# Performance work log

Hardware: AMD Instinct MI355X
Metric: run time of the kernel (lower is better)

Reference implementation:

```python
import jax, jax.numpy as jnp
import numpy as np

N, E, D_IN, HID = 100000, 3200000, 256, 128
EPS = 1e-5  # BatchNorm1d default eps


def batchnorm(x, gamma, beta):
    # training-mode BatchNorm1d: batch stats, biased variance
    mu = x.mean(axis=0)
    var = ((x - mu) ** 2).mean(axis=0)
    return (x - mu) * jax.lax.rsqrt(var + EPS) * gamma + beta


def setup_inputs() -> dict:
    key = jax.random.key(0)
    ks = jax.random.split(key, 6)
    s_in = 1.0 / np.sqrt(D_IN)
    s_h = 1.0 / np.sqrt(HID)
    return {
        "x": jax.random.normal(ks[0], (N, D_IN), jnp.float32),
        "edge_index": jax.random.randint(ks[1], (2, E), 0, N),
        "W1": jax.random.uniform(ks[2], (D_IN, HID), jnp.float32, -s_in, s_in),
        "b1": jnp.zeros((HID,), jnp.float32),
        "g1": jnp.ones((HID,), jnp.float32),
        "be1": jnp.zeros((HID,), jnp.float32),
        "Wl": jax.random.uniform(ks[3], (HID, HID), jnp.float32, -s_h, s_h),
        "bl": jnp.zeros((HID,), jnp.float32),
        "Wr": jax.random.uniform(ks[4], (HID, HID), jnp.float32, -s_h, s_h),
        "g2": jnp.ones((HID,), jnp.float32),
        "be2": jnp.zeros((HID,), jnp.float32),
    }


def reference(x, edge_index, W1, b1, g1, be1, Wl, bl, Wr, g2, be2):
    # input_linear: Linear -> BatchNorm1d, then ReLU
    feat = jax.nn.relu(batchnorm(x @ W1 + b1, g1, be1))  # [N, HID]

    # SAGEConv: mean-aggregate source features at destinations
    src, dst = edge_index[0], edge_index[1]
    msg_sum = jax.ops.segment_sum(feat[src], dst, num_segments=N)       # [N, HID]
    deg = jax.ops.segment_sum(jnp.ones((E, 1), feat.dtype), dst, num_segments=N)
    mean = msg_sum / jnp.maximum(deg, 1.0)

    # out = lin_l(aggr) + lin_r(x); lin_l has bias, lin_r does not (PyG default)
    out = mean @ Wl + bl + feat @ Wr
    out_feat = batchnorm(out, g2, be2)
    return feat, out_feat
```

## Files before the change

### kernel.cpp

```cpp
#include <hip/hip_runtime.h>

#define NN 100000
#define NE 3200000
#define KD 256
#define HD 128
#define NB 782
#define CAP 4608

typedef __bf16 bf16x8 __attribute__((ext_vector_type(8)));
typedef float  f32x8  __attribute__((ext_vector_type(8)));
typedef float  f32x4  __attribute__((ext_vector_type(4)));
typedef float  f32x2  __attribute__((ext_vector_type(2)));
typedef unsigned u32x2 __attribute__((ext_vector_type(2)));
typedef unsigned u32x4 __attribute__((ext_vector_type(4)));

__device__ __forceinline__ f32x4 mfma16(bf16x8 a, bf16x8 b, f32x4 c) {
  return __builtin_amdgcn_mfma_f32_16x16x32_bf16(a, b, c, 0, 0, 0);
}

__global__ void prep_w(const float* __restrict__ W1, const float* __restrict__ Wl,
                       const float* __restrict__ Wr, __bf16* __restrict__ Bt1,
                       __bf16* __restrict__ Bt2, float* __restrict__ stats,
                       int* __restrict__ bucket_cur) {
  if (blockIdx.x == 0) {
    for (int i = threadIdx.x; i < 1024; i += 256) stats[i] = 0.f;
  } else if (blockIdx.x == 1) {
    for (int i = threadIdx.x; i < NB; i += 256) bucket_cur[i] = i * CAP;
  }
  int c = blockIdx.x;
  int k = threadIdx.x;
  Bt1[c * KD + k] = (__bf16)W1[k * HD + c];
  float w = (k < HD) ? Wl[k * HD + c] : Wr[(k - HD) * HD + c];
  Bt2[c * KD + k] = (__bf16)w;
}

__global__ __launch_bounds__(1024) void b_scatter(const int* __restrict__ src,
                                                  const int* __restrict__ dst,
                                                  int* __restrict__ bucket_cur,
                                                  unsigned* __restrict__ pairs) {
  __shared__ int h[NB];
  __shared__ int cur[NB];
  __shared__ int gbase[NB];
  for (int i = threadIdx.x; i < NB; i += 1024) { h[i] = 0; cur[i] = 0; }
  __syncthreads();
  int base = blockIdx.x * 12500;
  for (int i = threadIdx.x; i < 12500; i += 1024)
    atomicAdd(&h[dst[base + i] >> 7], 1);
  __syncthreads();
  for (int b = threadIdx.x; b < NB; b += 1024) {
    int c = h[b];
    gbase[b] = c ? atomicAdd(&bucket_cur[b], c) : 0;
  }
  __syncthreads();
  for (int i = threadIdx.x; i < 12500; i += 1024) {
    int d = dst[base + i];
    int s = src[base + i];
    int b = d >> 7;
    int r = atomicAdd(&cur[b], 1);
    pairs[gbase[b] + r] = ((unsigned)s << 7) | (unsigned)(d & 127);
  }
}

__global__ __launch_bounds__(256) void b_sort(const int* __restrict__ bucket_cur,
                                              unsigned* __restrict__ pc,
                                              int* __restrict__ row_start,
                                              int* __restrict__ row_cnt) {
  __shared__ unsigned sin[CAP];
  __shared__ unsigned sout[CAP];
  __shared__ int h[128], ex[128];
  int b = blockIdx.x;
  int n0 = b * CAP;
  int cnt = bucket_cur[b] - n0;
  if (cnt > CAP) cnt = CAP;
  if (threadIdx.x < 128) h[threadIdx.x] = 0;
  __syncthreads();
  for (int i = threadIdx.x; i < cnt; i += 256) {
    unsigned v = pc[n0 + i];
    sin[i] = v;
    atomicAdd(&h[v & 127], 1);
  }
  __syncthreads();
  if (threadIdx.x < 128) ex[threadIdx.x] = h[threadIdx.x];
  __syncthreads();
  for (int off = 1; off < 128; off <<= 1) {
    int u = 0;
    if (threadIdx.x < 128 && threadIdx.x >= off) u = ex[threadIdx.x - off];
    __syncthreads();
    if (threadIdx.x < 128) ex[threadIdx.x] += u;
    __syncthreads();
  }
  if (threadIdx.x < 128) {
    int c = h[threadIdx.x];
    int excl = ex[threadIdx.x] - c;
    int node = b * 128 + threadIdx.x;
    if (node < NN) {
      row_start[node] = n0 + excl;
      row_cnt[node] = c;
    }
    h[threadIdx.x] = excl;
  }
  __syncthreads();
  for (int i = threadIdx.x; i < cnt; i += 256) {
    unsigned v = sin[i];
    int r = atomicAdd(&h[v & 127], 1);
    sout[r] = v >> 7;
  }
  __syncthreads();
  for (int i = threadIdx.x; i < cnt; i += 256)
    pc[n0 + i] = sout[i];
}

__global__ __launch_bounds__(256, 2) void gemm_x(const float* __restrict__ A,
                                                 const __bf16* __restrict__ Bt,
                                                 float* __restrict__ C,
                                                 float* __restrict__ sumc,
                                                 float* __restrict__ sqc) {
  __shared__ __bf16 sB[HD * KD];
  __shared__ float lsum[HD], lsq[HD];
  int tid = threadIdx.x;
  if (tid < HD) { lsum[tid] = 0.f; lsq[tid] = 0.f; }
  int wave = tid >> 6, lane = tid & 63;
  int q = lane >> 4, m = lane & 15;
  int rowbase = blockIdx.x * 256 + wave * 64;
  for (int i = tid; i < HD * KD / 8; i += 256) {
    int r = i >> 5, g = i & 31;
    bf16x8 v = *(const bf16x8*)(Bt + (size_t)r * KD + (g << 3));
    *(bf16x8*)(&sB[r * KD + ((g ^ (r & 7)) << 3)]) = v;
  }
  bf16x8 areg[4][8];
#pragma unroll
  for (int g = 0; g < 4; ++g) {
    int r = rowbase + g * 16 + m;
    if (r > NN - 1) r = NN - 1;
    const float* pa = A + (size_t)r * KD + q * 8;
    f32x8 u[8];
#pragma unroll
    for (int k = 0; k < 8; ++k) u[k] = *(const f32x8*)(pa + k * 32);
#pragma unroll
    for (int k = 0; k < 8; ++k) areg[g][k] = __builtin_convertvector(u[k], bf16x8);
  }
  __syncthreads();
#pragma unroll
  for (int hh = 0; hh < 2; ++hh) {
    f32x4 acc[4][4];
    f32x4 z = {0.f, 0.f, 0.f, 0.f};
#pragma unroll
    for (int g = 0; g < 4; ++g)
#pragma unroll
      for (int t = 0; t < 4; ++t) acc[g][t] = z;
#pragma unroll
    for (int ks = 0; ks < 8; ++ks) {
      int gb = ks * 4 + q;
#pragma unroll
      for (int t = 0; t < 4; ++t) {
        int c = hh * 64 + t * 16 + m;
        bf16x8 bb = *(const bf16x8*)(&sB[c * KD + ((gb ^ (c & 7)) << 3)]);
#pragma unroll
        for (int g = 0; g < 4; ++g) acc[g][t] = mfma16(areg[g][ks], bb, acc[g][t]);
      }
    }
    float ps[4], pq2[4];
#pragma unroll
    for (int t = 0; t < 4; ++t) { ps[t] = 0.f; pq2[t] = 0.f; }
#pragma unroll
    for (int g = 0; g < 4; ++g)
#pragma unroll
      for (int rg = 0; rg < 4; ++rg) {
        int r = rowbase + g * 16 + q * 4 + rg;
        if (r < NN) {
          float* Cr = C + (size_t)r * HD + hh * 64 + m;
#pragma unroll
          for (int t = 0; t < 4; ++t) {
            float v = acc[g][t][rg];
            Cr[t * 16] = v;
            ps[t] += v;
            pq2[t] += v * v;
          }
        }
      }
#pragma unroll
    for (int t = 0; t < 4; ++t) {
      atomicAdd(&lsum[hh * 64 + t * 16 + m], ps[t]);
      atomicAdd(&lsq[hh * 64 + t * 16 + m], pq2[t]);
    }
  }
  __syncthreads();
  if (tid < HD) {
    atomicAdd(&sumc[tid], lsum[tid]);
    atomicAdd(&sqc[tid], lsq[tid]);
  }
}

__global__ __launch_bounds__(256, 2) void gemm_cat(const __bf16* __restrict__ A0,
                                                   const __bf16* __restrict__ A1,
                                                   const __bf16* __restrict__ Bt,
                                                   float* __restrict__ C,
                                                   float* __restrict__ sumc,
                                                   float* __restrict__ sqc) {
  __shared__ __bf16 sB[HD * KD];
  __shared__ float lsum[HD], lsq[HD];
  int tid = threadIdx.x;
  if (tid < HD) { lsum[tid] = 0.f; lsq[tid] = 0.f; }
  int wave = tid >> 6, lane = tid & 63;
  int q = lane >> 4, m = lane & 15;
  int rowbase = blockIdx.x * 256 + wave * 64;
  for (int i = tid; i < HD * KD / 8; i += 256) {
    int r = i >> 5, g = i & 31;
    bf16x8 v = *(const bf16x8*)(Bt + (size_t)r * KD + (g << 3));
    *(bf16x8*)(&sB[r * KD + ((g ^ (r & 7)) << 3)]) = v;
  }
  bf16x8 areg[4][8];
#pragma unroll
  for (int g = 0; g < 4; ++g) {
    int r = rowbase + g * 16 + m;
    if (r > NN - 1) r = NN - 1;
    const __bf16* p0 = A0 + (size_t)r * HD + q * 8;
    const __bf16* p1 = A1 + (size_t)r * HD + q * 8;
#pragma unroll
    for (int k = 0; k < 4; ++k) areg[g][k] = *(const bf16x8*)(p0 + k * 32);
#pragma unroll
    for (int k = 0; k < 4; ++k) areg[g][4 + k] = *(const bf16x8*)(p1 + k * 32);
  }
  __syncthreads();
#pragma unroll
  for (int hh = 0; hh < 2; ++hh) {
    f32x4 acc[4][4];
    f32x4 z = {0.f, 0.f, 0.f, 0.f};
#pragma unroll
    for (int g = 0; g < 4; ++g)
#pragma unroll
      for (int t = 0; t < 4; ++t) acc[g][t] = z;
#pragma unroll
    for (int ks = 0; ks < 8; ++ks) {
      int gb = ks * 4 + q;
#pragma unroll
      for (int t = 0; t < 4; ++t) {
        int c = hh * 64 + t * 16 + m;
        bf16x8 bb = *(const bf16x8*)(&sB[c * KD + ((gb ^ (c & 7)) << 3)]);
#pragma unroll
        for (int g = 0; g < 4; ++g) acc[g][t] = mfma16(areg[g][ks], bb, acc[g][t]);
      }
    }
    float ps[4], pq2[4];
#pragma unroll
    for (int t = 0; t < 4; ++t) { ps[t] = 0.f; pq2[t] = 0.f; }
#pragma unroll
    for (int g = 0; g < 4; ++g)
#pragma unroll
      for (int rg = 0; rg < 4; ++rg) {
        int r = rowbase + g * 16 + q * 4 + rg;
        if (r < NN) {
          float* Cr = C + (size_t)r * HD + hh * 64 + m;
#pragma unroll
          for (int t = 0; t < 4; ++t) {
            float v = acc[g][t][rg];
            Cr[t * 16] = v;
            ps[t] += v;
            pq2[t] += v * v;
          }
        }
      }
#pragma unroll
    for (int t = 0; t < 4; ++t) {
      atomicAdd(&lsum[hh * 64 + t * 16 + m], ps[t]);
      atomicAdd(&lsq[hh * 64 + t * 16 + m], pq2[t]);
    }
  }
  __syncthreads();
  if (tid < HD) {
    atomicAdd(&sumc[tid], lsum[tid]);
    atomicAdd(&sqc[tid], lsq[tid]);
  }
}

__global__ __launch_bounds__(256) void bn_apply(const float* __restrict__ X,
                                                const float* __restrict__ sumc,
                                                const float* __restrict__ sqc,
                                                const float* __restrict__ g,
                                                const float* __restrict__ be,
                                                float* __restrict__ outf,
                                                __bf16* __restrict__ outb,
                                                unsigned char* __restrict__ outq,
                                                int relu) {
  __shared__ float sc[HD], sh[HD];
  if (threadIdx.x < HD) {
    int c = threadIdx.x;
    float mu = sumc[c] * (1.0f / NN);
    float var = sqc[c] * (1.0f / NN) - mu * mu;
    float rs = rsqrtf(var + 1e-5f);
    float a = rs * g[c];
    sc[c] = a;
    sh[c] = be[c] - mu * a;
  }
  __syncthreads();
  size_t base = ((size_t)blockIdx.x * 256 + threadIdx.x) * 8;
  int c0 = (int)(base & (HD - 1));
  f32x4 x0 = *(const f32x4*)(X + base);
  f32x4 x1 = *(const f32x4*)(X + base + 4);
  float o[8];
#pragma unroll
  for (int j = 0; j < 8; ++j) {
    float xv = (j < 4) ? x0[j] : x1[j - 4];
    float v = xv * sc[c0 + j] + sh[c0 + j];
    if (relu) v = fmaxf(v, 0.f);
    o[j] = v;
  }
  f32x4 o0 = {o[0], o[1], o[2], o[3]};
  f32x4 o1 = {o[4], o[5], o[6], o[7]};
  *(f32x4*)(outf + base) = o0;
  *(f32x4*)(outf + base + 4) = o1;
  if (outb) {
    bf16x8 ob;
#pragma unroll
    for (int j = 0; j < 8; ++j) ob[j] = (__bf16)o[j];
    *(bf16x8*)(outb + base) = ob;
    int w0 = 0, w1 = 0;
    w0 = __builtin_amdgcn_cvt_pk_fp8_f32(o[0], o[1], w0, false);
    w0 = __builtin_amdgcn_cvt_pk_fp8_f32(o[2], o[3], w0, true);
    w1 = __builtin_amdgcn_cvt_pk_fp8_f32(o[4], o[5], w1, false);
    w1 = __builtin_amdgcn_cvt_pk_fp8_f32(o[6], o[7], w1, true);
    u32x2 qv = {(unsigned)w0, (unsigned)w1};
    *(u32x2*)(outq + base) = qv;
  }
}

__global__ __launch_bounds__(256) void aggregate(const int* __restrict__ row_start,
                                                 const int* __restrict__ row_cnt,
                                                 const unsigned* __restrict__ csr,
                                                 const unsigned char* __restrict__ featq,
                                                 __bf16* __restrict__ meanb) {
  int node = blockIdx.x * 4 + (threadIdx.x >> 6);
  if (node >= NN) return;
  int lane = threadIdx.x & 63;
  int sub = lane >> 3;
  int m = lane & 7;
  int s = row_start[node];
  int deg = row_cnt[node];
  int e = s + deg;
  f32x2 acc[8];
#pragma unroll
  for (int j = 0; j < 8; ++j) acc[j] = (f32x2){0.f, 0.f};
  const u32x4* rows = (const u32x4*)featq;
  for (int base = s; base < e; base += 64) {
    int nb = e - base;
    if (nb > 64) nb = 64;
    unsigned my = 0;
    if (lane < nb) my = csr[base + lane];
#pragma unroll
    for (int t = 0; t < 64; t += 8) {
      int slot = t + sub;
      unsigned sn = __shfl(my, slot, 64);
      if (slot < nb) {
        u32x4 v = rows[(size_t)sn * 8 + m];
        acc[0] += __builtin_amdgcn_cvt_pk_f32_fp8((int)v.x, false);
        acc[1] += __builtin_amdgcn_cvt_pk_f32_fp8((int)v.x, true);
        acc[2] += __builtin_amdgcn_cvt_pk_f32_fp8((int)v.y, false);
        acc[3] += __builtin_amdgcn_cvt_pk_f32_fp8((int)v.y, true);
        acc[4] += __builtin_amdgcn_cvt_pk_f32_fp8((int)v.z, false);
        acc[5] += __builtin_amdgcn_cvt_pk_f32_fp8((int)v.z, true);
        acc[6] += __builtin_amdgcn_cvt_pk_f32_fp8((int)v.w, false);
        acc[7] += __builtin_amdgcn_cvt_pk_f32_fp8((int)v.w, true);
      }
    }
  }
#pragma unroll
  for (int j = 0; j < 8; ++j) {
    acc[j].x += __shfl_xor(acc[j].x, 8, 64);
    acc[j].y += __shfl_xor(acc[j].y, 8, 64);
    acc[j].x += __shfl_xor(acc[j].x, 16, 64);
    acc[j].y += __shfl_xor(acc[j].y, 16, 64);
    acc[j].x += __shfl_xor(acc[j].x, 32, 64);
    acc[j].y += __shfl_xor(acc[j].y, 32, 64);
  }
  if (sub == 0) {
    float inv = 1.0f / (float)(deg < 1 ? 1 : deg);
    bf16x8 o0, o1;
#pragma unroll
    for (int j = 0; j < 4; ++j) {
      o0[2 * j]     = (__bf16)(acc[j].x * inv);
      o0[2 * j + 1] = (__bf16)(acc[j].y * inv);
      o1[2 * j]     = (__bf16)(acc[4 + j].x * inv);
      o1[2 * j + 1] = (__bf16)(acc[4 + j].y * inv);
    }
    __bf16* dst = meanb + (size_t)node * HD + m * 16;
    *(bf16x8*)dst = o0;
    *(bf16x8*)(dst + 8) = o1;
  }
}

extern "C" void kernel_launch(void* const* d_in, const int* in_sizes, int n_in,
                              void* d_out, int out_size, void* d_ws, size_t ws_size,
                              hipStream_t stream) {
  (void)in_sizes; (void)n_in; (void)out_size; (void)ws_size;
  const float* x   = (const float*)d_in[0];
  const int*   ei  = (const int*)d_in[1];
  const float* W1  = (const float*)d_in[2];
  const float* g1  = (const float*)d_in[4];
  const float* be1 = (const float*)d_in[5];
  const float* Wl  = (const float*)d_in[6];
  const float* Wr  = (const float*)d_in[8];
  const float* g2  = (const float*)d_in[9];
  const float* be2 = (const float*)d_in[10];

  float* feat_out = (float*)d_out;
  float* out_feat = feat_out + (size_t)NN * HD;
  unsigned char* featq = (unsigned char*)out_feat;

  char* w = (char*)d_ws;
  float*    h          = (float*)(w);
  __bf16*   featb      = (__bf16*)(w + 51200000);
  __bf16*   meanb      = (__bf16*)(w + 76800000);
  unsigned* pc         = (unsigned*)(w + 102400000);
  int*      row_start  = (int*)(w + 116814848);
  int*      row_cnt    = (int*)(w + 117214848);
  int*      bucket_cur = (int*)(w + 117614848);
  float*    stats      = (float*)(w + 117618944);
  __bf16*   Bt1        = (__bf16*)(w + 117623040);
  __bf16*   Bt2        = (__bf16*)(w + 117688576);

  float* sum1 = stats,       * sq1 = stats + 128;
  float* sum2 = stats + 512, * sq2 = stats + 640;

  const int* esrc = ei;
  const int* edst = ei + NE;

  prep_w<<<128, 256, 0, stream>>>(W1, Wl, Wr, Bt1, Bt2, stats, bucket_cur);
  b_scatter<<<256, 1024, 0, stream>>>(esrc, edst, bucket_cur, pc);
  b_sort<<<NB, 256, 0, stream>>>(bucket_cur, pc, row_start, row_cnt);

  gemm_x<<<391, 256, 0, stream>>>(x, Bt1, h, sum1, sq1);
  bn_apply<<<6250, 256, 0, stream>>>(h, sum1, sq1, g1, be1, feat_out, featb, featq, 1);

  aggregate<<<25000, 256, 0, stream>>>(row_start, row_cnt, pc, featq, meanb);

  gemm_cat<<<391, 256, 0, stream>>>(meanb, featb, Bt2, h, sum2, sq2);
  bn_apply<<<6250, 256, 0, stream>>>(h, sum2, sq2, g2, be2, out_feat,
                                     (__bf16*)nullptr, (unsigned char*)nullptr, 0);
}
```

Measured before the change: 435.1 us.

## Store GEMM intermediates in bf16 and restructure gather to one node-row per wave

The pre-BatchNorm GEMM outputs are now written and read back as bf16 instead of fp32, which halves the traffic for that intermediate buffer. BN statistics are still accumulated from the fp32 accumulators, but the normalized values are computed from rounded inputs, which lowers precision. The mean-aggregation kernel is also rewritten so each wave reads whole 128-byte fp8 neighbor rows, two bytes per lane, using readlane broadcasts and eight loads in flight. This replaces the previous sub-group split, its u32x4 loads and the cross-lane shuffle reduction.

```diff
diff --git a/kernel.cpp b/kernel.cpp
--- a/kernel.cpp
+++ b/kernel.cpp
@@ -112,7 +112,7 @@
 
 __global__ __launch_bounds__(256, 2) void gemm_x(const float* __restrict__ A,
                                                  const __bf16* __restrict__ Bt,
-                                                 float* __restrict__ C,
+                                                 __bf16* __restrict__ C,
                                                  float* __restrict__ sumc,
                                                  float* __restrict__ sqc) {
   __shared__ __bf16 sB[HD * KD];
@@ -168,11 +168,11 @@
       for (int rg = 0; rg < 4; ++rg) {
         int r = rowbase + g * 16 + q * 4 + rg;
         if (r < NN) {
-          float* Cr = C + (size_t)r * HD + hh * 64 + m;
+          __bf16* Cr = C + (size_t)r * HD + hh * 64 + m;
 #pragma unroll
           for (int t = 0; t < 4; ++t) {
             float v = acc[g][t][rg];
-            Cr[t * 16] = v;
+            Cr[t * 16] = (__bf16)v;
             ps[t] += v;
             pq2[t] += v * v;
           }
@@ -194,7 +194,7 @@
 __global__ __launch_bounds__(256, 2) void gemm_cat(const __bf16* __restrict__ A0,
                                                    const __bf16* __restrict__ A1,
                                                    const __bf16* __restrict__ Bt,
-                                                   float* __restrict__ C,
+                                                   __bf16* __restrict__ C,
                                                    float* __restrict__ sumc,
                                                    float* __restrict__ sqc) {
   __shared__ __bf16 sB[HD * KD];
@@ -250,11 +250,11 @@
       for (int rg = 0; rg < 4; ++rg) {
         int r = rowbase + g * 16 + q * 4 + rg;
         if (r < NN) {
-          float* Cr = C + (size_t)r * HD + hh * 64 + m;
+          __bf16* Cr = C + (size_t)r * HD + hh * 64 + m;
 #pragma unroll
           for (int t = 0; t < 4; ++t) {
             float v = acc[g][t][rg];
-            Cr[t * 16] = v;
+            Cr[t * 16] = (__bf16)v;
             ps[t] += v;
             pq2[t] += v * v;
           }
@@ -273,7 +273,7 @@
   }
 }
 
-__global__ __launch_bounds__(256) void bn_apply(const float* __restrict__ X,
+__global__ __launch_bounds__(256) void bn_apply(const __bf16* __restrict__ X,
                                                 const float* __restrict__ sumc,
                                                 const float* __restrict__ sqc,
                                                 const float* __restrict__ g,
@@ -295,13 +295,11 @@
   __syncthreads();
   size_t base = ((size_t)blockIdx.x * 256 + threadIdx.x) * 8;
   int c0 = (int)(base & (HD - 1));
-  f32x4 x0 = *(const f32x4*)(X + base);
-  f32x4 x1 = *(const f32x4*)(X + base + 4);
+  bf16x8 xv = *(const bf16x8*)(X + base);
   float o[8];
 #pragma unroll
   for (int j = 0; j < 8; ++j) {
-    float xv = (j < 4) ? x0[j] : x1[j - 4];
-    float v = xv * sc[c0 + j] + sh[c0 + j];
+    float v = (float)xv[j] * sc[c0 + j] + sh[c0 + j];
     if (relu) v = fmaxf(v, 0.f);
     o[j] = v;
   }
@@ -332,60 +330,38 @@
   int node = blockIdx.x * 4 + (threadIdx.x >> 6);
   if (node >= NN) return;
   int lane = threadIdx.x & 63;
-  int sub = lane >> 3;
-  int m = lane & 7;
   int s = row_start[node];
   int deg = row_cnt[node];
   int e = s + deg;
-  f32x2 acc[8];
-#pragma unroll
-  for (int j = 0; j < 8; ++j) acc[j] = (f32x2){0.f, 0.f};
-  const u32x4* rows = (const u32x4*)featq;
+  f32x2 acc = {0.f, 0.f};
+  unsigned loff = (unsigned)lane * 2u;
   for (int base = s; base < e; base += 64) {
     int nb = e - base;
     if (nb > 64) nb = 64;
-    unsigned my = 0;
-    if (lane < nb) my = csr[base + lane];
-#pragma unroll
-    for (int t = 0; t < 64; t += 8) {
-      int slot = t + sub;
-      unsigned sn = __shfl(my, slot, 64);
-      if (slot < nb) {
-        u32x4 v = rows[(size_t)sn * 8 + m];
-        acc[0] += __builtin_amdgcn_cvt_pk_f32_fp8((int)v.x, false);
-        acc[1] += __builtin_amdgcn_cvt_pk_f32_fp8((int)v.x, true);
-        acc[2] += __builtin_amdgcn_cvt_pk_f32_fp8((int)v.y, false);
-        acc[3] += __builtin_amdgcn_cvt_pk_f32_fp8((int)v.y, true);
-        acc[4] += __builtin_amdgcn_cvt_pk_f32_fp8((int)v.z, false);
-        acc[5] += __builtin_amdgcn_cvt_pk_f32_fp8((int)v.z, true);
-        acc[6] += __builtin_amdgcn_cvt_pk_f32_fp8((int)v.w, false);
-        acc[7] += __builtin_amdgcn_cvt_pk_f32_fp8((int)v.w, true);
+    unsigned my = (lane < nb) ? csr[base + lane] : 0u;
+    int g8 = nb & ~7;
+    for (int t = 0; t < g8; t += 8) {
+      unsigned vv[8];
+#pragma unroll
+      for (int j = 0; j < 8; ++j) {
+        unsigned sn = (unsigned)__builtin_amdgcn_readlane((int)my, t + j);
+        vv[j] = *(const unsigned short*)(featq + (((size_t)sn << 7) + loff));
       }
-    }
-  }
-#pragma unroll
-  for (int j = 0; j < 8; ++j) {
-    acc[j].x += __shfl_xor(acc[j].x, 8, 64);
-    acc[j].y += __shfl_xor(acc[j].y, 8, 64);
-    acc[j].x += __shfl_xor(acc[j].x, 16, 64);
-    acc[j].y += __shfl_xor(acc[j].y, 16, 64);
-    acc[j].x += __shfl_xor(acc[j].x, 32, 64);
-    acc[j].y += __shfl_xor(acc[j].y, 32, 64);
-  }
-  if (sub == 0) {
-    float inv = 1.0f / (float)(deg < 1 ? 1 : deg);
-    bf16x8 o0, o1;
-#pragma unroll
-    for (int j = 0; j < 4; ++j) {
-      o0[2 * j]     = (__bf16)(acc[j].x * inv);
-      o0[2 * j + 1] = (__bf16)(acc[j].y * inv);
-      o1[2 * j]     = (__bf16)(acc[4 + j].x * inv);
-      o1[2 * j + 1] = (__bf16)(acc[4 + j].y * inv);
-    }
-    __bf16* dst = meanb + (size_t)node * HD + m * 16;
-    *(bf16x8*)dst = o0;
-    *(bf16x8*)(dst + 8) = o1;
-  }
+#pragma unroll
+      for (int j = 0; j < 8; ++j)
+        acc += __builtin_amdgcn_cvt_pk_f32_fp8((int)vv[j], false);
+    }
+    for (int t = g8; t < nb; ++t) {
+      unsigned sn = (unsigned)__builtin_amdgcn_readlane((int)my, t);
+      unsigned v = *(const unsigned short*)(featq + (((size_t)sn << 7) + loff));
+      acc += __builtin_amdgcn_cvt_pk_f32_fp8((int)v, false);
+    }
+  }
+  float inv = 1.0f / (float)(deg < 1 ? 1 : deg);
+  union { unsigned u; __bf16 b[2]; } pk;
+  pk.b[0] = (__bf16)(acc.x * inv);
+  pk.b[1] = (__bf16)(acc.y * inv);
+  *(unsigned*)(meanb + (size_t)node * HD + lane * 2) = pk.u;
 }
 
 extern "C" void kernel_launch(void* const* d_in, const int* in_sizes, int n_in,
@@ -407,7 +383,7 @@
   unsigned char* featq = (unsigned char*)out_feat;
 
   char* w = (char*)d_ws;
-  float*    h          = (float*)(w);
+  __bf16*   h          = (__bf16*)(w);
   __bf16*   featb      = (__bf16*)(w + 51200000);
   __bf16*   meanb      = (__bf16*)(w + 76800000);
   unsigned* pc         = (unsigned*)(w + 102400000);
```

After: 424.7 us. 2.4% less time.
